# Optimization experiments

Measured on AMD Instinct MI355X. Metric: run time of the kernel, lower is better.

The kernel has to match this reference:

```python
import jax, jax.numpy as jnp
import numpy as np

H = 256            # hidden size per layer
NUM_LAYERS = 3
IN_SIZE = 256
GATE_COLS = 4 * H + 1   # f, i, o, g, z_tilde


def _hard_sigm(x):
    return jnp.clip((x + 1.0) * 0.5, 0.0, 1.0)


def _st_binarize(z_hat):
    # straight-through: hard round in fwd, hard-sigmoid grad in bwd
    return z_hat + jax.lax.stop_gradient(jnp.round(z_hat) - z_hat)


def _cell(Wb, Wr, Wt, b, h_bottom, h, h_top, c, z, z_bottom):
    # HM-LSTM cell: bottom-up input gated by z_bottom, top-down gated by own previous z
    s = z_bottom * (h_bottom @ Wb) + h @ Wr + z * (h_top @ Wt) + b
    f = jax.nn.sigmoid(s[:, 0 * H:1 * H])
    i = jax.nn.sigmoid(s[:, 1 * H:2 * H])
    o = jax.nn.sigmoid(s[:, 2 * H:3 * H])
    g = jnp.tanh(s[:, 3 * H:4 * H])
    z_new = _st_binarize(_hard_sigm(s[:, 4 * H:4 * H + 1]))
    # flush (own z=1): c=i*g ; update (z=0, z_bottom=1): f*c+i*g ; copy: c
    c_new = z * (i * g) + (1.0 - z) * (z_bottom * (f * c + i * g) + (1.0 - z_bottom) * c)
    copy = (1.0 - z) * (1.0 - z_bottom)
    h_new = copy * h + (1.0 - copy) * (o * jnp.tanh(c_new))
    return h_new, c_new, z_new


def _forward(x, params):
    B, T, _ = x.shape
    hs0 = [jnp.zeros((B, H), x.dtype) for _ in range(NUM_LAYERS)]
    cs0 = [jnp.zeros((B, H), x.dtype) for _ in range(NUM_LAYERS)]
    zs0 = [jnp.zeros((B, 1), x.dtype) for _ in range(NUM_LAYERS)]
    h_top_last = jnp.zeros((B, 1), x.dtype)  # top layer sees a zero h_top of size 1
    ones = jnp.ones((B, 1), x.dtype)

    def step(carry, x_t):
        hs, cs, zs = carry
        h_bottom, z_bottom = x_t, ones  # layer 0 always receives z_bottom=1
        hs_n, cs_n, zs_n = [], [], []
        for l in range(NUM_LAYERS):
            Wb, Wr, Wt, b = params[l]
            h_top = hs[l + 1] if l + 1 < NUM_LAYERS else h_top_last  # delayed top-down (t-1)
            h_new, c_new, z_new = _cell(Wb, Wr, Wt, b, h_bottom, hs[l], h_top, cs[l], zs[l], z_bottom)
            hs_n.append(h_new); cs_n.append(c_new); zs_n.append(z_new)
            h_bottom, z_bottom = h_new, z_new
        h_cat = jnp.concatenate(hs_n, axis=1)  # (B, L*H)
        z_cat = jnp.concatenate(zs_n, axis=1)  # (B, L)
        return (hs_n, cs_n, zs_n), (h_cat, z_cat)

    x_t_first = jnp.swapaxes(x, 0, 1)  # (T, B, In)
    _, (h_all, z_all) = jax.lax.scan(step, (hs0, cs0, zs0), x_t_first)
    return jnp.swapaxes(h_all, 0, 1), jnp.swapaxes(z_all, 0, 1)


def setup_inputs() -> dict:
    key = jax.random.key(0)
    ks = jax.random.split(key, 1 + 4 * NUM_LAYERS)
    x = jax.random.normal(ks[0], (64, 512, IN_SIZE), dtype=jnp.float32)
    out = {"x": x}
    ki = 1
    for l in range(NUM_LAYERS):
        bot = IN_SIZE if l == 0 else H
        top = 1 if l + 1 == NUM_LAYERS else H
        out[f"Wb{l}"] = jax.random.normal(ks[ki], (bot, GATE_COLS), dtype=jnp.float32) * 0.05; ki += 1
        out[f"Wr{l}"] = jax.random.normal(ks[ki], (H, GATE_COLS), dtype=jnp.float32) * 0.05; ki += 1
        out[f"Wt{l}"] = jax.random.normal(ks[ki], (top, GATE_COLS), dtype=jnp.float32) * 0.05; ki += 1
        out[f"b{l}"] = jax.random.normal(ks[ki], (GATE_COLS,), dtype=jnp.float32) * 0.05; ki += 1
    return out


def reference(x, Wb0, Wr0, Wt0, b0, Wb1, Wr1, Wt1, b1, Wb2, Wr2, Wt2, b2):
    params = [(Wb0, Wr0, Wt0, b0), (Wb1, Wr1, Wt1, b1), (Wb2, Wr2, Wt2, b2)]
    return _forward(x, params)
```

## Files before the change

kernel.cpp:

```cpp
#include <hip/hip_runtime.h>
#include <cmath>


#define Hh    256
#define Bb    64
#define Tt    512
#define GC    1025
#define NGRP  32
#define RPG   2
#define WDOG  400000
#define WBOOT 2000000

__device__ __forceinline__ void g_st(float* p, float v) {
    __hip_atomic_store(p, v, __ATOMIC_RELAXED, __HIP_MEMORY_SCOPE_AGENT);
}
__device__ __forceinline__ float g_ldf(const float* p) {
    return __hip_atomic_load(p, __ATOMIC_RELAXED, __HIP_MEMORY_SCOPE_AGENT);
}
__device__ __forceinline__ unsigned int a_add(unsigned int* p, unsigned int v) {
    return __hip_atomic_fetch_add(p, v, __ATOMIC_RELAXED, __HIP_MEMORY_SCOPE_AGENT);
}
__device__ __forceinline__ unsigned int a_ld32(const unsigned int* p) {
    return __hip_atomic_load(p, __ATOMIC_RELAXED, __HIP_MEMORY_SCOPE_AGENT);
}
__device__ __forceinline__ unsigned int xcc_id() {
    unsigned int x;
    asm("s_getreg_b32 %0, hwreg(HW_REG_XCC_ID)" : "=s"(x));
    return x & 7u;
}

struct WSrc { const float* wb[3]; const float* wr[3]; const float* wt[3]; };

__global__ __launch_bounds__(256) void build_w4s(WSrc S, float* __restrict__ w4s,
                                                 float* __restrict__ wz) {
    const int gk = blockIdx.x;
    int l, k;
    if (gk < 768)       { l = 0; k = gk; }
    else if (gk < 1536) { l = 1; k = gk - 768; }
    else                { l = 2; k = gk - 1536; }
    const float* src;
    if (k < 256)      src = S.wb[l] + (size_t)k * GC;
    else if (k < 512) src = S.wr[l] + (size_t)(k - 256) * GC;
    else              src = S.wt[l] + (size_t)(k - 512) * GC;
#pragma unroll
    for (int it = 0; it < 4; ++it) {
        const int idx = it * 256 + threadIdx.x;
        const int s  = idx >> 7;
        const int cl = idx & 127;
        const int scol = (cl >> 5) * 256 + s * 32 + (cl & 31);
        w4s[((((size_t)s * 3 + l) * 192 + (k >> 2)) * 128 + cl) * 4 + (k & 3)] = src[scol];
    }
    if (threadIdx.x == 0) wz[l * 768 + k] = src[1024];
}

struct PK {
    const float* x;
    const float* w4s;
    const float* wz;
    const float* bias[3];
    float* zws;
    unsigned int* bar;
    unsigned int* asn;
    float* out_h;
    float* out_z;
};

__global__ __launch_bounds__(512, 1) void chain_kernel(PK P) {
    __shared__ float A[768 * RPG];
    __shared__ float red[8][128][3];
    __shared__ float zbS[RPG], zoS[RPG];
    __shared__ unsigned int sRole;
    __shared__ float ballast[17920];

    const int tid   = threadIdx.x;
    const int lane  = tid & 63;
    const int wave  = tid >> 6;

    if (P.out_h == nullptr) {
        ballast[tid] = (float)tid;
        g_st(&P.out_z[tid], ballast[tid ^ 1]);
    }

    if (tid == 0) {
        const unsigned int x = xcc_id();
        const unsigned int idx = a_add(&P.asn[x * 32], 1u);
        a_add(&P.asn[512], 1u);
        int it = 0;
        while (a_ld32(&P.asn[512]) < 256u && it < WBOOT) { __builtin_amdgcn_s_sleep(8); ++it; }
        bool bal = (it < WBOOT) && (idx < 32u);
        if (bal) {
#pragma unroll
            for (int q = 0; q < 8; ++q)
                if (a_ld32(&P.asn[q * 32]) != 32u) bal = false;
        }
        sRole = bal ? (idx * 8u + x)
                    : ((unsigned)(blockIdx.x >> 3) * 8u + (blockIdx.x & 7));
    }
    __syncthreads();
    const int group = sRole >> 3;
    const int shard = sRole & 7;
    const int row0  = group * RPG;

    unsigned int* grpCnt = P.bar + group * 32;
    unsigned int stage = 0;
    bool broken = false;

    float creg[3] = {0.f, 0.f, 0.f};
    float hreg[3] = {0.f, 0.f, 0.f};

    const int gi0 = lane >> 5;
    const int jl  = lane & 31;
    const int cl0 = gi0 * 32 + jl;
    const int cl1 = (gi0 + 2) * 32 + jl;

    for (int t = 0; t < Tt; ++t) {
#pragma unroll
        for (int l = 0; l < 3; ++l) {
            const int K = (l < 2) ? 768 : 512;
            const float* __restrict__ bias = P.bias[l];

            if (tid < RPG) {
                const int r = row0 + tid;
                float zo = (t > 0) ? g_ldf(&P.zws[((size_t)r * 1539 + ((t - 1) * 3 + l)) * 32]) : 0.f;
                float zb = (l == 0) ? 1.f
                         : g_ldf(&P.zws[((size_t)r * 1539 + (t * 3 + l - 1)) * 32]);
                zoS[tid] = zo; zbS[tid] = zb;
            }
            __syncthreads();

            for (int e = tid; e < RPG * K; e += 512) {
                const int row = (e < K) ? 0 : 1;
                const int k   = e - row * K;
                const int r   = row0 + row;
                float v;
                if (k < 256) {
                    float b = (l == 0)
                        ? P.x[((size_t)r * Tt + t) * 256 + k]
                        : g_ldf(&P.out_h[((size_t)r * Tt + t) * 768 + (l - 1) * 256 + k]);
                    v = zbS[row] * b;
                } else if (k < 512) {
                    v = (t > 0)
                        ? g_ldf(&P.out_h[((size_t)r * Tt + (t - 1)) * 768 + l * 256 + (k - 256)])
                        : 0.f;
                } else {
                    float tp = (t > 0)
                        ? g_ldf(&P.out_h[((size_t)r * Tt + (t - 1)) * 768 + (l + 1) * 256 + (k - 512)])
                        : 0.f;
                    v = zoS[row] * tp;
                }
                A[k * RPG + row] = v;
            }
            __syncthreads();

            {
                const int Kb  = K >> 5;
                const int kb0 = wave * Kb;
                const float4* __restrict__ W4ls =
                    (const float4*)P.w4s + ((size_t)shard * 3 + l) * 192 * 128;
                float acc0[RPG], acc1[RPG];
#pragma unroll
                for (int r = 0; r < RPG; ++r) { acc0[r] = 0.f; acc1[r] = 0.f; }
                for (int kb = kb0; kb < kb0 + Kb; ++kb) {
                    float4 w0 = W4ls[(size_t)kb * 128 + cl0];
                    float4 w1 = W4ls[(size_t)kb * 128 + cl1];
#pragma unroll
                    for (int q = 0; q < 4; ++q) {
                        float2 a = *(const float2*)&A[(kb * 4 + q) * RPG];
                        const float wq0 = (&w0.x)[q];
                        const float wq1 = (&w1.x)[q];
                        acc0[0] += wq0 * a.x; acc0[1] += wq0 * a.y;
                        acc1[0] += wq1 * a.x; acc1[1] += wq1 * a.y;
                    }
                }
#pragma unroll
                for (int r = 0; r < RPG; ++r) red[wave][cl0][r] = acc0[r];
#pragma unroll
                for (int r = 0; r < RPG; ++r) red[wave][cl1][r] = acc1[r];
            }

            if (shard == 7 && wave < RPG) {
                const float* __restrict__ wzl = P.wz + l * 768;
                double zp = 0.0;
                for (int k = lane; k < K; k += 64)
                    zp += (double)wzl[k] * (double)A[k * RPG + wave];
#pragma unroll
                for (int off = 32; off > 0; off >>= 1)
                    zp += __shfl_down(zp, off);
                if (lane == 0) {
                    double s = (double)bias[1024] + zp;
                    float znew = (s > 0.0) ? 1.0f : 0.0f;
                    const int r = row0 + wave;
                    g_st(&P.zws[((size_t)r * 1539 + (t * 3 + l)) * 32], znew);
                    P.out_z[((size_t)r * Tt + t) * 3 + l] = znew;
                }
            }
            __syncthreads();

            if (tid < RPG * 32) {
                const int row = tid >> 5;
                const int j   = tid & 31;
                const int r   = row0 + row;
                float s0 = bias[0 * Hh + shard * 32 + j];
                float s1 = bias[1 * Hh + shard * 32 + j];
                float s2 = bias[2 * Hh + shard * 32 + j];
                float s3 = bias[3 * Hh + shard * 32 + j];
#pragma unroll
                for (int w = 0; w < 8; ++w) {
                    s0 += red[w][0 * 32 + j][row];
                    s1 += red[w][1 * 32 + j][row];
                    s2 += red[w][2 * 32 + j][row];
                    s3 += red[w][3 * 32 + j][row];
                }
                float f = 1.0f / (1.0f + expf(-s0));
                float i = 1.0f / (1.0f + expf(-s1));
                float o = 1.0f / (1.0f + expf(-s2));
                float g = tanhf(s3);
                float zb_ = zbS[row];
                float zo_ = zoS[row];
                float c    = creg[l];
                float hold = hreg[l];
                float ig   = i * g;
                float cupd = f * c + ig;
                float cnew = (zo_ != 0.0f) ? ig : ((zb_ != 0.0f) ? cupd : c);
                float hnew = (zo_ == 0.0f && zb_ == 0.0f) ? hold : (o * tanhf(cnew));
                creg[l] = cnew;
                hreg[l] = hnew;
                g_st(&P.out_h[((size_t)r * Tt + t) * 768 + l * 256 + shard * 32 + j], hnew);
            }

            __syncthreads();
            if (tid == 0) {
                a_add(grpCnt, 1u);
                if (!broken) {
                    const unsigned int tgt = 8u * (stage + 1u);
                    unsigned int v = 0; int it = 0;
                    for (; it < WDOG; ++it) {
                        v = a_ld32(grpCnt);
                        if (v >= tgt) break;
                        __builtin_amdgcn_s_sleep(2);
                    }
                    broken = (v < tgt);
                }
            }
            __syncthreads();
            ++stage;
        }
    }
}

extern "C" void kernel_launch(void* const* d_in, const int* in_sizes, int n_in,
                              void* d_out, int out_size, void* d_ws, size_t ws_size,
                              hipStream_t stream) {
    (void)in_sizes; (void)n_in; (void)out_size;

    const float* x = (const float*)d_in[0];
    float* wsf = (float*)d_ws;

    const size_t OFF_W4  = 0;
    const size_t OFF_WZ  = OFF_W4 + (size_t)8 * 3 * 192 * 128 * 4;
    const size_t OFF_ZWS = OFF_WZ + 3 * 768 + 64;
    const size_t OFF_BAR = OFF_ZWS + (size_t)64 * 1539 * 32;
    const size_t OFF_ASN = OFF_BAR + 1024;
    const size_t OFF_END = OFF_ASN + 1024;

    float* w4s = wsf + OFF_W4;
    float* wz  = wsf + OFF_WZ;
    float* zws = wsf + OFF_ZWS;
    unsigned int* bar = (unsigned int*)(wsf + OFF_BAR);
    unsigned int* asn = (unsigned int*)(wsf + OFF_ASN);

    if (ws_size < OFF_END * sizeof(float)) return;

    hipMemsetAsync(bar, 0, 2048 * sizeof(float), stream);

    WSrc S;
    S.wb[0] = (const float*)d_in[1];  S.wr[0] = (const float*)d_in[2];  S.wt[0] = (const float*)d_in[3];
    S.wb[1] = (const float*)d_in[5];  S.wr[1] = (const float*)d_in[6];  S.wt[1] = (const float*)d_in[7];
    S.wb[2] = (const float*)d_in[9];  S.wr[2] = (const float*)d_in[10]; S.wt[2] = (const float*)d_in[11];
    build_w4s<<<2048, 256, 0, stream>>>(S, w4s, wz);

    PK pk;
    pk.x = x;
    pk.w4s = w4s;
    pk.wz = wz;
    pk.bias[0] = (const float*)d_in[4];
    pk.bias[1] = (const float*)d_in[8];
    pk.bias[2] = (const float*)d_in[12];
    pk.zws = zws;
    pk.bar = bar;
    pk.asn = asn;
    pk.out_h = (float*)d_out;
    pk.out_z = (float*)d_out + (size_t)Bb * Tt * 768;

    chain_kernel<<<256, 512, 0, stream>>>(pk);
}
```

Measured before the change: 10.87 ms.

## Double-buffer the gate input vector and prefetch next stage's recurrent operands

The shared input vector A is split into two buffers. The recurrent and top-down parts of the next layer/timestep input are gathered into the spare buffer while the current matvec runs, since they depend only on already-published hidden states. Only the bottom-up part, which depends on the layer just computed, stays on the serial critical path. This reduces latency-exposed global loads per stage, at the cost of extra LDS, which is offset by shrinking the ballast array.

After: 8.706 ms (median of 2 runs). -19.9%, faster.

```diff
diff --git a/kernel.cpp b/kernel.cpp
--- a/kernel.cpp
+++ b/kernel.cpp
@@ -66,11 +66,12 @@
 };
 
 __global__ __launch_bounds__(512, 1) void chain_kernel(PK P) {
-    __shared__ float A[768 * RPG];
+    __shared__ float A0[768 * RPG];
+    __shared__ float A1[768 * RPG];
     __shared__ float red[8][128][3];
-    __shared__ float zbS[RPG], zoS[RPG];
+    __shared__ float zbS[RPG], zoS[RPG], zoN[RPG];
     __shared__ unsigned int sRole;
-    __shared__ float ballast[17920];
+    __shared__ float ballast[14848];
 
     const int tid   = threadIdx.x;
     const int lane  = tid & 63;
@@ -113,11 +114,26 @@
     const int cl0 = gi0 * 32 + jl;
     const int cl1 = (gi0 + 2) * 32 + jl;
 
+    float* Acur = A0;
+    float* Anxt = A1;
+
+    {
+        const int row = tid >> 8;
+        const int kq  = tid & 255;
+        const int r   = row0 + row;
+        A0[kq * RPG + row]         = P.x[((size_t)r * Tt + 0) * 256 + kq];
+        A0[(256 + kq) * RPG + row] = 0.f;
+        A0[(512 + kq) * RPG + row] = 0.f;
+    }
+
     for (int t = 0; t < Tt; ++t) {
 #pragma unroll
         for (int l = 0; l < 3; ++l) {
             const int K = (l < 2) ? 768 : 512;
             const float* __restrict__ bias = P.bias[l];
+            const bool hasNext = !(t == Tt - 1 && l == 2);
+            const int tn = (l < 2) ? t : t + 1;
+            const int ln = (l < 2) ? l + 1 : 0;
 
             if (tid < RPG) {
                 const int r = row0 + tid;
@@ -125,32 +141,39 @@
                 float zb = (l == 0) ? 1.f
                          : g_ldf(&P.zws[((size_t)r * 1539 + (t * 3 + l - 1)) * 32]);
                 zoS[tid] = zo; zbS[tid] = zb;
-            }
-            __syncthreads();
-
-            for (int e = tid; e < RPG * K; e += 512) {
-                const int row = (e < K) ? 0 : 1;
-                const int k   = e - row * K;
+            } else if (tid < 2 * RPG) {
+                const int row = tid - RPG;
+                const int r = row0 + row;
+                zoN[row] = (hasNext && tn > 0)
+                    ? g_ldf(&P.zws[((size_t)r * 1539 + ((tn - 1) * 3 + ln)) * 32]) : 0.f;
+            }
+            __syncthreads();
+
+            if (l > 0) {
+                const int row = tid >> 8;
+                const int kq  = tid & 255;
                 const int r   = row0 + row;
-                float v;
-                if (k < 256) {
-                    float b = (l == 0)
-                        ? P.x[((size_t)r * Tt + t) * 256 + k]
-                        : g_ldf(&P.out_h[((size_t)r * Tt + t) * 768 + (l - 1) * 256 + k]);
-                    v = zbS[row] * b;
-                } else if (k < 512) {
-                    v = (t > 0)
-                        ? g_ldf(&P.out_h[((size_t)r * Tt + (t - 1)) * 768 + l * 256 + (k - 256)])
+                float b = g_ldf(&P.out_h[((size_t)r * Tt + t) * 768 + (l - 1) * 256 + kq]);
+                Acur[kq * RPG + row] = zbS[row] * b;
+            }
+            __syncthreads();
+
+            if (hasNext) {
+                const int row = tid >> 8;
+                const int kq  = tid & 255;
+                const int r   = row0 + row;
+                float vr = (tn > 0)
+                    ? g_ldf(&P.out_h[((size_t)r * Tt + (tn - 1)) * 768 + ln * 256 + kq]) : 0.f;
+                Anxt[(256 + kq) * RPG + row] = vr;
+                if (ln < 2) {
+                    float vt = (tn > 0)
+                        ? zoN[row] * g_ldf(&P.out_h[((size_t)r * Tt + (tn - 1)) * 768 + (ln + 1) * 256 + kq])
                         : 0.f;
-                } else {
-                    float tp = (t > 0)
-                        ? g_ldf(&P.out_h[((size_t)r * Tt + (t - 1)) * 768 + (l + 1) * 256 + (k - 512)])
-                        : 0.f;
-                    v = zoS[row] * tp;
-                }
-                A[k * RPG + row] = v;
-            }
-            __syncthreads();
+                    Anxt[(512 + kq) * RPG + row] = vt;
+                }
+                if (ln == 0)
+                    Anxt[kq * RPG + row] = P.x[((size_t)r * Tt + tn) * 256 + kq];
+            }
 
             {
                 const int Kb  = K >> 5;
@@ -165,7 +188,7 @@
                     float4 w1 = W4ls[(size_t)kb * 128 + cl1];
 #pragma unroll
                     for (int q = 0; q < 4; ++q) {
-                        float2 a = *(const float2*)&A[(kb * 4 + q) * RPG];
+                        float2 a = *(const float2*)&Acur[(kb * 4 + q) * RPG];
                         const float wq0 = (&w0.x)[q];
                         const float wq1 = (&w1.x)[q];
                         acc0[0] += wq0 * a.x; acc0[1] += wq0 * a.y;
@@ -182,7 +205,7 @@
                 const float* __restrict__ wzl = P.wz + l * 768;
                 double zp = 0.0;
                 for (int k = lane; k < K; k += 64)
-                    zp += (double)wzl[k] * (double)A[k * RPG + wave];
+                    zp += (double)wzl[k] * (double)Acur[k * RPG + wave];
 #pragma unroll
                 for (int off = 32; off > 0; off >>= 1)
                     zp += __shfl_down(zp, off);
@@ -244,6 +267,8 @@
             }
             __syncthreads();
             ++stage;
+
+            float* tmp = Acur; Acur = Anxt; Anxt = tmp;
         }
     }
 }
```
